# Performance work log

Hardware: AMD Instinct MI355X
Metric: run time of the kernel (lower is better)

Reference implementation:

```python
import jax, jax.numpy as jnp
import numpy as np

N = 8192
IN_F = 512
OUT_F = 256


def mish(x):
    return x * jnp.tanh(jax.nn.softplus(x))


def setup_inputs() -> dict:
    key = jax.random.key(0)
    k1, k2, k3, k4 = jax.random.split(key, 4)
    inp = jax.random.normal(k1, (N, IN_F), dtype=jnp.float32)
    # random binary adjacency mask (float, used via adj > 0), ensure self-loops
    adj = jax.random.randint(k2, (N, N), 0, 2).astype(jnp.float32)
    adj = adj.at[jnp.arange(N), jnp.arange(N)].set(1.0)
    # xavier_uniform_ init
    lim_W = float(np.sqrt(6.0 / (IN_F + OUT_F)))
    W = jax.random.uniform(k3, (IN_F, OUT_F), minval=-lim_W, maxval=lim_W, dtype=jnp.float32)
    lim_a = float(np.sqrt(6.0 / (2 * OUT_F + 1)))
    a = jax.random.uniform(k4, (2 * OUT_F, 1), minval=-lim_a, maxval=lim_a, dtype=jnp.float32)
    return {"input": inp, "adj": adj, "W": W, "a": a}


def reference(input, adj, W, a):
    # h: [N, F_out]
    h = input @ W
    f_out = W.shape[1]
    a1 = a[:f_out, 0]   # applied to source node (row i)
    a2 = a[f_out:, 0]   # applied to target node (col j)
    # e[i, j] = mish(h_i . a1 + h_j . a2)  -- identical math to the
    # O(N^2*2F) concat([h_i, h_j]) @ a in the torch reference.
    e = mish((h @ a1)[:, None] + (h @ a2)[None, :])  # [N, N]
    attention = jnp.where(adj > 0, e, jnp.float32(-9e15))
    attention = jax.nn.softmax(attention, axis=1)
    # dropout is inference-off (training=False)
    h_prime = attention @ h  # [N, F_out]
    return mish(h_prime)
```

## Files before the change

### kernel.cpp

```cpp
#include <hip/hip_runtime.h>

typedef __attribute__((ext_vector_type(8))) short short8;
typedef __attribute__((ext_vector_type(4))) float f32x4;

#define L2E 1.44269504088896340736f

__device__ __forceinline__ unsigned short f2bf(float x) {
    union { float f; unsigned int u; } v; v.f = x;
    unsigned int u = v.u;
    unsigned int r = (u + 0x7FFFu + ((u >> 16) & 1u)) >> 16;
    return (unsigned short)r;
}

__device__ __forceinline__ float mishf(float x) {
    float u = __builtin_amdgcn_exp2f(x * L2E);
    float t = u * (u + 2.0f);
    return x * t * __builtin_amdgcn_rcpf(t + 2.0f);
}

__device__ __forceinline__ short pw(float aj, float sv, float ev, float s1Lv, float e1v) {
    float xL = s1Lv + sv;
    float u  = e1v * ev;
    float t  = u * (u + 2.0f);
    float m  = xL * t * __builtin_amdgcn_rcpf(t + 2.0f);
    float p  = aj * __builtin_amdgcn_exp2f(m);
    union { float f; unsigned int u; } b; b.f = p;
    return (short)((b.u + 0x8000u) >> 16);
}

typedef __attribute__((address_space(1))) const unsigned int guint;
typedef __attribute__((address_space(3))) unsigned int luint;
__device__ __forceinline__ void lds16(const void* g, void* l) {
    __builtin_amdgcn_global_load_lds((guint*)g, (luint*)l, 16, 0, 0);
}

__global__ void k_cvt_wt(const float* __restrict__ W, unsigned short* __restrict__ wt) {
    int c = blockIdx.x;
    int t = threadIdx.x;
    wt[c * 512 + t]       = f2bf(W[(size_t)t * 256 + c]);
    wt[c * 512 + t + 256] = f2bf(W[(size_t)(t + 256) * 256 + c]);
}

__global__ __launch_bounds__(64) void k_gemm_h(const float* __restrict__ input,
                                               const unsigned short* __restrict__ wt,
                                               const float* __restrict__ a,
                                               unsigned short* __restrict__ hbt,
                                               float* __restrict__ s1L,
                                               float* __restrict__ s2L,
                                               float* __restrict__ e2) {
    int lane = threadIdx.x & 63, g = lane >> 4, r = lane & 15;
    int base = blockIdx.x * 16;

    f32x4 acc[16];
#pragma unroll
    for (int n = 0; n < 16; ++n) acc[n] = (f32x4)0.0f;

    const float* arow = input + (size_t)(base + r) * 512 + g * 8;
#pragma unroll 2
    for (int kb = 0; kb < 512; kb += 32) {
        float4 a0 = *(const float4*)(arow + kb);
        float4 a1 = *(const float4*)(arow + kb + 4);
        short8 af;
        af[0] = (short)f2bf(a0.x); af[1] = (short)f2bf(a0.y);
        af[2] = (short)f2bf(a0.z); af[3] = (short)f2bf(a0.w);
        af[4] = (short)f2bf(a1.x); af[5] = (short)f2bf(a1.y);
        af[6] = (short)f2bf(a1.z); af[7] = (short)f2bf(a1.w);
#pragma unroll
        for (int n = 0; n < 16; ++n) {
            short8 bf = *(const short8*)(wt + (size_t)(n * 16 + r) * 512 + kb + g * 8);
            acc[n] = __builtin_amdgcn_mfma_f32_16x16x32_bf16(af, bf, acc[n], 0, 0, 0);
        }
    }
    int rowc = base + g * 4;
#pragma unroll
    for (int n = 0; n < 16; ++n) {
        int col = n * 16 + r;
        ushort4 pk;
        pk.x = f2bf(acc[n][0]); pk.y = f2bf(acc[n][1]);
        pk.z = f2bf(acc[n][2]); pk.w = f2bf(acc[n][3]);
        *(ushort4*)(hbt + (size_t)col * 8192 + rowc) = pk;
    }
    float p1[4] = {0,0,0,0}, p2[4] = {0,0,0,0};
#pragma unroll
    for (int n = 0; n < 16; ++n) {
        float a1v = a[n * 16 + r];
        float a2v = a[256 + n * 16 + r];
#pragma unroll
        for (int i = 0; i < 4; ++i) {
            p1[i] += acc[n][i] * a1v;
            p2[i] += acc[n][i] * a2v;
        }
    }
#pragma unroll
    for (int off = 8; off >= 1; off >>= 1) {
#pragma unroll
        for (int i = 0; i < 4; ++i) {
            p1[i] += __shfl_xor(p1[i], off);
            p2[i] += __shfl_xor(p2[i], off);
        }
    }
    if (r == 0) {
#pragma unroll
        for (int i = 0; i < 4; ++i) {
            int row = rowc + i;
            s1L[row] = p1[i] * L2E;
            float s2l = p2[i] * L2E;
            s2L[row] = s2l;
            e2[row] = __builtin_amdgcn_exp2f(s2l);
        }
    }
}

__global__ __launch_bounds__(256, 2) void k_attn(const float* __restrict__ adj,
                                                 const unsigned short* __restrict__ hbt,
                                                 const float* __restrict__ s1L,
                                                 const float* __restrict__ s2L,
                                                 const float* __restrict__ e2,
                                                 float* __restrict__ pS,
                                                 float* __restrict__ pZ) {
    __shared__ __align__(16) unsigned short tile[3][8192];

    int tid = threadIdx.x;
    int w = tid >> 6, lane = tid & 63, g = lane >> 4, r = lane & 15;
    int mb = blockIdx.x, chunk = blockIdx.y;
    int kc = chunk * 2048;
    int rowA = mb * 64 + w * 16 + r;
    float s1Lv = s1L[rowA];
    float e1v = __builtin_amdgcn_exp2f(s1Lv);

    const float* adjp = adj + (size_t)rowA * 8192 + kc + g * 8;
    const float* svp  = s2L + kc + g * 8;
    const float* evp  = e2  + kc + g * 8;

    const unsigned short *hsrc0, *hsrc1, *hsrc2, *hsrc3;
    {
        int l2 = lane >> 2, sl = lane & 3;
        int r0 = 64 * w + l2,      ss0 = sl ^ ((r0 >> 1) & 3);
        int r1 = 64 * w + 16 + l2, ss1 = sl ^ ((r1 >> 1) & 3);
        int r2 = 64 * w + 32 + l2, ss2 = sl ^ ((r2 >> 1) & 3);
        int r3 = 64 * w + 48 + l2, ss3 = sl ^ ((r3 >> 1) & 3);
        hsrc0 = hbt + (size_t)r0 * 8192 + kc + ss0 * 8;
        hsrc1 = hbt + (size_t)r1 * 8192 + kc + ss1 * 8;
        hsrc2 = hbt + (size_t)r2 * 8192 + kc + ss2 * 8;
        hsrc3 = hbt + (size_t)r3 * 8192 + kc + ss3 * 8;
    }
    char* ldsbase = (char*)&tile[0][0] + w * 4096;
    int sw = (r >> 1) & 3;
    int rdoff = r * 64 + ((g ^ sw) * 16);

    f32x4 acc[17];
#pragma unroll
    for (int n = 0; n < 17; ++n) acc[n] = (f32x4)0.0f;

    short8 onef;
    {
        short ov = (r == 0) ? (short)0x3F80 : (short)0;
#pragma unroll
        for (int j = 0; j < 8; ++j) onef[j] = ov;
    }

    float4 ajA0, ajA1, svA0, svA1, evA0, evA1;
    float4 ajB0, ajB1, svB0, svB1, evB0, evB1;

#define ISSUE(tt, bufn, AJ0, AJ1, SV0, SV1, EV0, EV1) do {                     \
        int t_ = (tt); if (t_ > 63) t_ = 63;                                   \
        int ko_ = t_ * 32;                                                     \
        char* lb_ = ldsbase + (bufn) * 16384;                                  \
        lds16(hsrc0 + ko_, lb_);                                               \
        lds16(hsrc1 + ko_, lb_ + 1024);                                        \
        lds16(hsrc2 + ko_, lb_ + 2048);                                        \
        lds16(hsrc3 + ko_, lb_ + 3072);                                        \
        AJ0 = *(const float4*)(adjp + ko_);                                    \
        AJ1 = *(const float4*)(adjp + ko_ + 4);                                \
        SV0 = *(const float4*)(svp + ko_);                                     \
        SV1 = *(const float4*)(svp + ko_ + 4);                                 \
        EV0 = *(const float4*)(evp + ko_);                                     \
        EV1 = *(const float4*)(evp + ko_ + 4);                                 \
    } while (0)

#define WAITBAR() do {                                                         \
        asm volatile("s_waitcnt vmcnt(10)" ::: "memory");                      \
        __builtin_amdgcn_sched_barrier(0);                                     \
        __builtin_amdgcn_s_barrier();                                          \
        __builtin_amdgcn_sched_barrier(0);                                     \
    } while (0)

#define COMPUTE(bufc, AJ0, AJ1, SV0, SV1, EV0, EV1) do {                       \
        short8 af_;                                                            \
        af_[0] = pw(AJ0.x, SV0.x, EV0.x, s1Lv, e1v);                           \
        af_[1] = pw(AJ0.y, SV0.y, EV0.y, s1Lv, e1v);                           \
        af_[2] = pw(AJ0.z, SV0.z, EV0.z, s1Lv, e1v);                           \
        af_[3] = pw(AJ0.w, SV0.w, EV0.w, s1Lv, e1v);                           \
        af_[4] = pw(AJ1.x, SV1.x, EV1.x, s1Lv, e1v);                           \
        af_[5] = pw(AJ1.y, SV1.y, EV1.y, s1Lv, e1v);                           \
        af_[6] = pw(AJ1.z, SV1.z, EV1.z, s1Lv, e1v);                           \
        af_[7] = pw(AJ1.w, SV1.w, EV1.w, s1Lv, e1v);                           \
        const char* tb_ = (const char*)&tile[0][0] + (bufc) * 16384 + rdoff;   \
        _Pragma("unroll")                                                      \
        for (int n_ = 0; n_ < 16; ++n_) {                                      \
            short8 bf_ = *(const short8*)(tb_ + n_ * 1024);                    \
            acc[n_] = __builtin_amdgcn_mfma_f32_16x16x32_bf16(af_, bf_, acc[n_], 0, 0, 0); \
        }                                                                      \
        acc[16] = __builtin_amdgcn_mfma_f32_16x16x32_bf16(af_, onef, acc[16], 0, 0, 0);    \
    } while (0)

    ISSUE(0, 0, ajA0, ajA1, svA0, svA1, evA0, evA1);

    int cur = 0;
    for (int s = 0; s < 64; s += 2) {
        int nb = cur + 1; if (nb == 3) nb = 0;
        ISSUE(s + 1, nb, ajB0, ajB1, svB0, svB1, evB0, evB1);
        WAITBAR();
        COMPUTE(cur, ajA0, ajA1, svA0, svA1, evA0, evA1);
        cur = nb; nb = cur + 1; if (nb == 3) nb = 0;
        ISSUE(s + 2, nb, ajA0, ajA1, svA0, svA1, evA0, evA1);
        WAITBAR();
        COMPUTE(cur, ajB0, ajB1, svB0, svB1, evB0, evB1);
        cur = nb;
    }

    float* ps = pS + ((size_t)chunk << 21);
    int rowc = mb * 64 + w * 16 + g * 4;
#pragma unroll
    for (int n = 0; n < 16; ++n) {
#pragma unroll
        for (int i = 0; i < 4; ++i)
            ps[(size_t)(rowc + i) * 256 + n * 16 + r] = acc[n][i];
    }
    if (r == 0) {
        float* pz = pZ + chunk * 8192 + rowc;
#pragma unroll
        for (int i = 0; i < 4; ++i) pz[i] = acc[16][i];
    }
#undef ISSUE
#undef WAITBAR
#undef COMPUTE
}

__global__ void k_final(const float* __restrict__ pS, const float* __restrict__ pZ,
                        float* __restrict__ out) {
    int i = blockIdx.x;
    int f = threadIdx.x;
    size_t o = (size_t)i * 256 + f;
    float sv = pS[o] + pS[o + (1u << 21)] + pS[o + (2u << 21)] + pS[o + (3u << 21)];
    float z = pZ[i] + pZ[i + 8192] + pZ[i + 16384] + pZ[i + 24576];
    float hp = sv / z;
    out[o] = mishf(hp);
}

extern "C" void kernel_launch(void* const* d_in, const int* in_sizes, int n_in,
                              void* d_out, int out_size, void* d_ws, size_t ws_size,
                              hipStream_t stream) {
    const float* input = (const float*)d_in[0];
    const float* adj   = (const float*)d_in[1];
    const float* W     = (const float*)d_in[2];
    const float* a     = (const float*)d_in[3];
    float* out = (float*)d_out;

    char* ws = (char*)d_ws;
    unsigned short* wt  = (unsigned short*)ws;
    unsigned short* hbt = (unsigned short*)(ws + 262144);
    float* s1L = (float*)(ws + 4456448);
    float* s2L = (float*)(ws + 4489216);
    float* e2  = (float*)(ws + 4521984);
    float* pS  = (float*)(ws + 4554752);
    float* pZ  = (float*)(ws + 38109184);

    hipLaunchKernelGGL(k_cvt_wt, dim3(256), dim3(256), 0, stream, W, wt);
    hipLaunchKernelGGL(k_gemm_h, dim3(512), dim3(64), 0, stream, input, wt, a, hbt, s1L, s2L, e2);
    hipLaunchKernelGGL(k_attn, dim3(128, 4), dim3(256), 0, stream, adj, hbt, s1L, s2L, e2, pS, pZ);
    hipLaunchKernelGGL(k_final, dim3(8192), dim3(256), 0, stream, pS, pZ, out);
}
```

Measured before the change: 460.1 us.

## Pack adjacency into bitmask, deepen LDS pipeline, split h GEMM across four waves

A new pre-pass reads the fp32 adjacency once and packs it into a per-row bitmask with wave ballots. The attention kernel then reads 32 bits per 32 columns instead of 32 floats, and it computes exp(s2) inline instead of loading a precomputed e2 array. The attention pipeline moves from three to four LDS buffers with a fixed 4-stage unrolled schedule and a lower vmcnt threshold. The h GEMM now spreads output columns across four waves per block and reduces the attention dot products through shared memory. The cost is one extra full pass over adj plus one more exp2 per element in the attention kernel.

```diff
diff --git a/kernel.cpp b/kernel.cpp
--- a/kernel.cpp
+++ b/kernel.cpp
@@ -18,20 +18,44 @@
     return x * t * __builtin_amdgcn_rcpf(t + 2.0f);
 }
 
-__device__ __forceinline__ short pw(float aj, float sv, float ev, float s1Lv, float e1v) {
-    float xL = s1Lv + sv;
-    float u  = e1v * ev;
-    float t  = u * (u + 2.0f);
-    float m  = xL * t * __builtin_amdgcn_rcpf(t + 2.0f);
-    float p  = aj * __builtin_amdgcn_exp2f(m);
+__device__ __forceinline__ short pw(unsigned int mb, int j, float sv, float s1v) {
+    float xL = s1v + sv;
+    float u = __builtin_amdgcn_exp2f(xL);
+    float t = u * (u + 2.0f);
+    float m = xL * t * __builtin_amdgcn_rcpf(t + 2.0f);
+    float p = __builtin_amdgcn_exp2f(m);
     union { float f; unsigned int u; } b; b.f = p;
-    return (short)((b.u + 0x8000u) >> 16);
+    unsigned short h = (unsigned short)((b.u + 0x8000u) >> 16);
+    return ((mb >> j) & 1u) ? (short)h : (short)0;
 }
 
 typedef __attribute__((address_space(1))) const unsigned int guint;
 typedef __attribute__((address_space(3))) unsigned int luint;
 __device__ __forceinline__ void lds16(const void* g, void* l) {
     __builtin_amdgcn_global_load_lds((guint*)g, (luint*)l, 16, 0, 0);
+}
+
+__global__ __launch_bounds__(256) void k_pack(const float* __restrict__ adj,
+                                              unsigned int* __restrict__ mask) {
+    int wid = blockIdx.x * 4 + (threadIdx.x >> 6);
+    int lane = threadIdx.x & 63;
+    const float* row = adj + (size_t)wid * 8192 + lane;
+    unsigned int* mrow = mask + wid * 256;
+#pragma unroll 2
+    for (int base = 0; base < 8192; base += 256) {
+        float v0 = row[base];
+        float v1 = row[base + 64];
+        float v2 = row[base + 128];
+        float v3 = row[base + 192];
+        unsigned long long b0 = __ballot(v0 > 0.5f);
+        unsigned long long b1 = __ballot(v1 > 0.5f);
+        unsigned long long b2 = __ballot(v2 > 0.5f);
+        unsigned long long b3 = __ballot(v3 > 0.5f);
+        if (lane == 0) {
+            *(ulonglong2*)(mrow + (base >> 5))     = make_ulonglong2(b0, b1);
+            *(ulonglong2*)(mrow + (base >> 5) + 4) = make_ulonglong2(b2, b3);
+        }
+    }
 }
 
 __global__ void k_cvt_wt(const float* __restrict__ W, unsigned short* __restrict__ wt) {
@@ -41,22 +65,24 @@
     wt[c * 512 + t + 256] = f2bf(W[(size_t)(t + 256) * 256 + c]);
 }
 
-__global__ __launch_bounds__(64) void k_gemm_h(const float* __restrict__ input,
-                                               const unsigned short* __restrict__ wt,
-                                               const float* __restrict__ a,
-                                               unsigned short* __restrict__ hbt,
-                                               float* __restrict__ s1L,
-                                               float* __restrict__ s2L,
-                                               float* __restrict__ e2) {
-    int lane = threadIdx.x & 63, g = lane >> 4, r = lane & 15;
+__global__ __launch_bounds__(256) void k_gemm_h(const float* __restrict__ input,
+                                                const unsigned short* __restrict__ wt,
+                                                const float* __restrict__ a,
+                                                unsigned short* __restrict__ hbt,
+                                                float* __restrict__ s1L,
+                                                float* __restrict__ s2L) {
+    __shared__ float red[2][4][16];
+    int tid = threadIdx.x;
+    int w = tid >> 6, lane = tid & 63, g = lane >> 4, r = lane & 15;
     int base = blockIdx.x * 16;
 
-    f32x4 acc[16];
-#pragma unroll
-    for (int n = 0; n < 16; ++n) acc[n] = (f32x4)0.0f;
+    f32x4 acc[4];
+#pragma unroll
+    for (int n = 0; n < 4; ++n) acc[n] = (f32x4)0.0f;
 
     const float* arow = input + (size_t)(base + r) * 512 + g * 8;
-#pragma unroll 2
+    const unsigned short* wp = wt + (size_t)(w * 64 + r) * 512 + g * 8;
+#pragma unroll 4
     for (int kb = 0; kb < 512; kb += 32) {
         float4 a0 = *(const float4*)(arow + kb);
         float4 a1 = *(const float4*)(arow + kb + 4);
@@ -66,29 +92,29 @@
         af[4] = (short)f2bf(a1.x); af[5] = (short)f2bf(a1.y);
         af[6] = (short)f2bf(a1.z); af[7] = (short)f2bf(a1.w);
 #pragma unroll
-        for (int n = 0; n < 16; ++n) {
-            short8 bf = *(const short8*)(wt + (size_t)(n * 16 + r) * 512 + kb + g * 8);
-            acc[n] = __builtin_amdgcn_mfma_f32_16x16x32_bf16(af, bf, acc[n], 0, 0, 0);
+        for (int n2 = 0; n2 < 4; ++n2) {
+            short8 bf = *(const short8*)(wp + n2 * 8192 + kb);
+            acc[n2] = __builtin_amdgcn_mfma_f32_16x16x32_bf16(af, bf, acc[n2], 0, 0, 0);
         }
     }
     int rowc = base + g * 4;
 #pragma unroll
-    for (int n = 0; n < 16; ++n) {
-        int col = n * 16 + r;
+    for (int n2 = 0; n2 < 4; ++n2) {
+        int col = w * 64 + n2 * 16 + r;
         ushort4 pk;
-        pk.x = f2bf(acc[n][0]); pk.y = f2bf(acc[n][1]);
-        pk.z = f2bf(acc[n][2]); pk.w = f2bf(acc[n][3]);
+        pk.x = f2bf(acc[n2][0]); pk.y = f2bf(acc[n2][1]);
+        pk.z = f2bf(acc[n2][2]); pk.w = f2bf(acc[n2][3]);
         *(ushort4*)(hbt + (size_t)col * 8192 + rowc) = pk;
     }
     float p1[4] = {0,0,0,0}, p2[4] = {0,0,0,0};
 #pragma unroll
-    for (int n = 0; n < 16; ++n) {
-        float a1v = a[n * 16 + r];
-        float a2v = a[256 + n * 16 + r];
+    for (int n2 = 0; n2 < 4; ++n2) {
+        float a1v = a[w * 64 + n2 * 16 + r];
+        float a2v = a[256 + w * 64 + n2 * 16 + r];
 #pragma unroll
         for (int i = 0; i < 4; ++i) {
-            p1[i] += acc[n][i] * a1v;
-            p2[i] += acc[n][i] * a2v;
+            p1[i] += acc[n2][i] * a1v;
+            p2[i] += acc[n2][i] * a2v;
         }
     }
 #pragma unroll
@@ -102,35 +128,36 @@
     if (r == 0) {
 #pragma unroll
         for (int i = 0; i < 4; ++i) {
-            int row = rowc + i;
-            s1L[row] = p1[i] * L2E;
-            float s2l = p2[i] * L2E;
-            s2L[row] = s2l;
-            e2[row] = __builtin_amdgcn_exp2f(s2l);
-        }
-    }
-}
-
-__global__ __launch_bounds__(256, 2) void k_attn(const float* __restrict__ adj,
+            red[0][w][g * 4 + i] = p1[i];
+            red[1][w][g * 4 + i] = p2[i];
+        }
+    }
+    __syncthreads();
+    if (tid < 16) {
+        float s1 = red[0][0][tid] + red[0][1][tid] + red[0][2][tid] + red[0][3][tid];
+        float s2 = red[1][0][tid] + red[1][1][tid] + red[1][2][tid] + red[1][3][tid];
+        s1L[base + tid] = s1 * L2E;
+        s2L[base + tid] = s2 * L2E;
+    }
+}
+
+__global__ __launch_bounds__(256, 2) void k_attn(const unsigned int* __restrict__ mask,
                                                  const unsigned short* __restrict__ hbt,
                                                  const float* __restrict__ s1L,
                                                  const float* __restrict__ s2L,
-                                                 const float* __restrict__ e2,
                                                  float* __restrict__ pS,
                                                  float* __restrict__ pZ) {
-    __shared__ __align__(16) unsigned short tile[3][8192];
+    __shared__ __align__(16) unsigned short tile[4][8192];
 
     int tid = threadIdx.x;
     int w = tid >> 6, lane = tid & 63, g = lane >> 4, r = lane & 15;
     int mb = blockIdx.x, chunk = blockIdx.y;
     int kc = chunk * 2048;
     int rowA = mb * 64 + w * 16 + r;
-    float s1Lv = s1L[rowA];
-    float e1v = __builtin_amdgcn_exp2f(s1Lv);
-
-    const float* adjp = adj + (size_t)rowA * 8192 + kc + g * 8;
-    const float* svp  = s2L + kc + g * 8;
-    const float* evp  = e2  + kc + g * 8;
+    float s1v = s1L[rowA];
+
+    const unsigned int* mkp = mask + (size_t)rowA * 256 + chunk * 64;
+    const float* svp = s2L + kc + g * 8;
 
     const unsigned short *hsrc0, *hsrc1, *hsrc2, *hsrc3;
     {
@@ -144,7 +171,6 @@
         hsrc2 = hbt + (size_t)r2 * 8192 + kc + ss2 * 8;
         hsrc3 = hbt + (size_t)r3 * 8192 + kc + ss3 * 8;
     }
-    char* ldsbase = (char*)&tile[0][0] + w * 4096;
     int sw = (r >> 1) & 3;
     int rdoff = r * 64 + ((g ^ sw) * 16);
 
@@ -159,42 +185,40 @@
         for (int j = 0; j < 8; ++j) onef[j] = ov;
     }
 
-    float4 ajA0, ajA1, svA0, svA1, evA0, evA1;
-    float4 ajB0, ajB1, svB0, svB1, evB0, evB1;
-
-#define ISSUE(tt, bufn, AJ0, AJ1, SV0, SV1, EV0, EV1) do {                     \
+    unsigned int mkA, mkB, mkC, mkD;
+    float4 svA0, svA1, svB0, svB1, svC0, svC1, svD0, svD1;
+
+#define ISSUE(tt, bufn, MK, SV0, SV1) do {                                     \
         int t_ = (tt); if (t_ > 63) t_ = 63;                                   \
         int ko_ = t_ * 32;                                                     \
-        char* lb_ = ldsbase + (bufn) * 16384;                                  \
+        char* lb_ = (char*)&tile[0][0] + (bufn) * 16384 + w * 4096;            \
         lds16(hsrc0 + ko_, lb_);                                               \
         lds16(hsrc1 + ko_, lb_ + 1024);                                        \
         lds16(hsrc2 + ko_, lb_ + 2048);                                        \
         lds16(hsrc3 + ko_, lb_ + 3072);                                        \
-        AJ0 = *(const float4*)(adjp + ko_);                                    \
-        AJ1 = *(const float4*)(adjp + ko_ + 4);                                \
+        MK = mkp[t_];                                                          \
         SV0 = *(const float4*)(svp + ko_);                                     \
         SV1 = *(const float4*)(svp + ko_ + 4);                                 \
-        EV0 = *(const float4*)(evp + ko_);                                     \
-        EV1 = *(const float4*)(evp + ko_ + 4);                                 \
     } while (0)
 
 #define WAITBAR() do {                                                         \
-        asm volatile("s_waitcnt vmcnt(10)" ::: "memory");                      \
+        asm volatile("s_waitcnt vmcnt(7)" ::: "memory");                       \
         __builtin_amdgcn_sched_barrier(0);                                     \
         __builtin_amdgcn_s_barrier();                                          \
         __builtin_amdgcn_sched_barrier(0);                                     \
     } while (0)
 
-#define COMPUTE(bufc, AJ0, AJ1, SV0, SV1, EV0, EV1) do {                       \
+#define COMPUTE(bufc, MK, SV0, SV1) do {                                       \
+        unsigned int mby_ = (MK) >> (g * 8);                                   \
         short8 af_;                                                            \
-        af_[0] = pw(AJ0.x, SV0.x, EV0.x, s1Lv, e1v);                           \
-        af_[1] = pw(AJ0.y, SV0.y, EV0.y, s1Lv, e1v);                           \
-        af_[2] = pw(AJ0.z, SV0.z, EV0.z, s1Lv, e1v);                           \
-        af_[3] = pw(AJ0.w, SV0.w, EV0.w, s1Lv, e1v);                           \
-        af_[4] = pw(AJ1.x, SV1.x, EV1.x, s1Lv, e1v);                           \
-        af_[5] = pw(AJ1.y, SV1.y, EV1.y, s1Lv, e1v);                           \
-        af_[6] = pw(AJ1.z, SV1.z, EV1.z, s1Lv, e1v);                           \
-        af_[7] = pw(AJ1.w, SV1.w, EV1.w, s1Lv, e1v);                           \
+        af_[0] = pw(mby_, 0, SV0.x, s1v);                                      \
+        af_[1] = pw(mby_, 1, SV0.y, s1v);                                      \
+        af_[2] = pw(mby_, 2, SV0.z, s1v);                                      \
+        af_[3] = pw(mby_, 3, SV0.w, s1v);                                      \
+        af_[4] = pw(mby_, 4, SV1.x, s1v);                                      \
+        af_[5] = pw(mby_, 5, SV1.y, s1v);                                      \
+        af_[6] = pw(mby_, 6, SV1.z, s1v);                                      \
+        af_[7] = pw(mby_, 7, SV1.w, s1v);                                      \
         const char* tb_ = (const char*)&tile[0][0] + (bufc) * 16384 + rdoff;   \
         _Pragma("unroll")                                                      \
         for (int n_ = 0; n_ < 16; ++n_) {                                      \
@@ -204,19 +228,22 @@
         acc[16] = __builtin_amdgcn_mfma_f32_16x16x32_bf16(af_, onef, acc[16], 0, 0, 0);    \
     } while (0)
 
-    ISSUE(0, 0, ajA0, ajA1, svA0, svA1, evA0, evA1);
-
-    int cur = 0;
-    for (int s = 0; s < 64; s += 2) {
-        int nb = cur + 1; if (nb == 3) nb = 0;
-        ISSUE(s + 1, nb, ajB0, ajB1, svB0, svB1, evB0, evB1);
+    ISSUE(0, 0, mkA, svA0, svA1);
+    ISSUE(1, 1, mkB, svB0, svB1);
+
+    for (int s = 0; s < 64; s += 4) {
         WAITBAR();
-        COMPUTE(cur, ajA0, ajA1, svA0, svA1, evA0, evA1);
-        cur = nb; nb = cur + 1; if (nb == 3) nb = 0;
-        ISSUE(s + 2, nb, ajA0, ajA1, svA0, svA1, evA0, evA1);
+        ISSUE(s + 2, 2, mkC, svC0, svC1);
+        COMPUTE(0, mkA, svA0, svA1);
         WAITBAR();
-        COMPUTE(cur, ajB0, ajB1, svB0, svB1, evB0, evB1);
-        cur = nb;
+        ISSUE(s + 3, 3, mkD, svD0, svD1);
+        COMPUTE(1, mkB, svB0, svB1);
+        WAITBAR();
+        ISSUE(s + 4, 0, mkA, svA0, svA1);
+        COMPUTE(2, mkC, svC0, svC1);
+        WAITBAR();
+        ISSUE(s + 5, 1, mkB, svB0, svB1);
+        COMPUTE(3, mkD, svD0, svD1);
     }
 
     float* ps = pS + ((size_t)chunk << 21);
@@ -258,16 +285,17 @@
     float* out = (float*)d_out;
 
     char* ws = (char*)d_ws;
-    unsigned short* wt  = (unsigned short*)ws;
-    unsigned short* hbt = (unsigned short*)(ws + 262144);
-    float* s1L = (float*)(ws + 4456448);
-    float* s2L = (float*)(ws + 4489216);
-    float* e2  = (float*)(ws + 4521984);
-    float* pS  = (float*)(ws + 4554752);
-    float* pZ  = (float*)(ws + 38109184);
-
+    unsigned short* wt   = (unsigned short*)ws;
+    unsigned short* hbt  = (unsigned short*)(ws + 262144);
+    float* s1L           = (float*)(ws + 4456448);
+    float* s2L           = (float*)(ws + 4489216);
+    unsigned int* mask   = (unsigned int*)(ws + 4521984);
+    float* pS            = (float*)(ws + 12910592);
+    float* pZ            = (float*)(ws + 46465024);
+
+    hipLaunchKernelGGL(k_pack, dim3(2048), dim3(256), 0, stream, adj, mask);
     hipLaunchKernelGGL(k_cvt_wt, dim3(256), dim3(256), 0, stream, W, wt);
-    hipLaunchKernelGGL(k_gemm_h, dim3(512), dim3(64), 0, stream, input, wt, a, hbt, s1L, s2L, e2);
-    hipLaunchKernelGGL(k_attn, dim3(128, 4), dim3(256), 0, stream, adj, hbt, s1L, s2L, e2, pS, pZ);
+    hipLaunchKernelGGL(k_gemm_h, dim3(512), dim3(256), 0, stream, input, wt, a, hbt, s1L, s2L);
+    hipLaunchKernelGGL(k_attn, dim3(128, 4), dim3(256), 0, stream, mask, hbt, s1L, s2L, pS, pZ);
     hipLaunchKernelGGL(k_final, dim3(8192), dim3(256), 0, stream, pS, pZ, out);
 }
```

Measured after the change: 480.2 us. 4.4% more time.
